# Kernel tuning notes

Hardware: AMD Instinct MI355X
Metric: run time of the kernel (lower is better)

The kernel has to match this reference:

```python
import jax, jax.numpy as jnp
import numpy as np

L, B, H, D, S, FF = 24, 4, 16, 512, 4096, 2048
HD = D // H
POS = 2048  # current kv_cache_len (write position)
EPS = 1e-5
SCALE = 1.0 / np.sqrt(HD)


def layer_norm(x, w, b):
    m = jnp.mean(x, axis=-1, keepdims=True)
    v = jnp.mean(jnp.square(x - m), axis=-1, keepdims=True)
    return (x - m) * jax.lax.rsqrt(v + EPS) * w + b


def setup_inputs() -> dict:
    key = jax.random.key(0)
    ks = jax.random.split(key, 12)
    f = lambda k, shape: jax.random.normal(k, shape, dtype=jnp.float32) * 0.02
    # decode mask: positions [0, POS] are attendable (index_fill_ sets POS True)
    attn_mask = jnp.broadcast_to(jnp.arange(S) <= POS, (B, H, 1, S))
    return {
        "x": jax.random.normal(ks[0], (B, 1, D), dtype=jnp.float32),
        "k_cache": jax.random.normal(ks[1], (L, B, H, S, HD), dtype=jnp.float32),
        "v_cache": jax.random.normal(ks[2], (L, B, H, S, HD), dtype=jnp.float32),
        "attn_mask": attn_mask,
        "qkv_w": f(ks[3], (L, 3 * D, D)),
        "qkv_b": f(ks[4], (L, 3 * D)),
        "out_w": f(ks[5], (L, D, D)),
        "out_b": f(ks[6], (L, D)),
        "mlp_w1": f(ks[7], (L, FF, D)),
        "mlp_b1": f(ks[8], (L, FF)),
        "mlp_w2": f(ks[9], (L, D, FF)),
        "mlp_b2": f(ks[10], (L, D)),
        "norm_w1": jnp.ones((L, D), jnp.float32),
        "norm_b1": jnp.zeros((L, D), jnp.float32),
        "norm_w2": jnp.ones((L, D), jnp.float32),
        "norm_b2": jnp.zeros((L, D), jnp.float32),
        "kv_cache_len": POS,
    }


def reference(x, k_cache, v_cache, attn_mask, qkv_w, qkv_b, out_w, out_b,
              mlp_w1, mlp_b1, mlp_w2, mlp_b2, norm_w1, norm_b1, norm_w2,
              norm_b2, kv_cache_len):
    pos = kv_cache_len

    def block(h, p):
        kc0, vc0, qw, qb, ow, ob, w1, b1, w2, b2, nw1, nb1, nw2, nb2 = p
        qkv = h @ qw.T + qb                      # [B,1,3D]
        q, k, v = jnp.split(qkv, 3, axis=-1)
        q = q.reshape(B, 1, H, HD).transpose(0, 2, 1, 3)   # [B,H,1,HD]
        k = k.reshape(B, 1, H, HD).transpose(0, 2, 1, 3)
        v = v.reshape(B, 1, H, HD).transpose(0, 2, 1, 3)
        # in-place cache update at write position (index_copy_ on dim 2)
        kc = kc0.at[:, :, pos, :].set(k[:, :, 0, :])       # [B,H,S,HD]
        vc = vc0.at[:, :, pos, :].set(v[:, :, 0, :])
        scores = jnp.einsum('bhqd,bhkd->bhqk', q, kc) * SCALE
        scores = jnp.where(attn_mask, scores, -1e9)
        attn = jnp.einsum('bhqk,bhkd->bhqd', jax.nn.softmax(scores, axis=-1), vc)
        attn = attn.transpose(0, 2, 1, 3).reshape(B, 1, D)
        attn = attn @ ow.T + ob
        h = layer_norm(h + attn, nw1, nb1)
        mlp = jax.nn.relu(h @ w1.T + b1) @ w2.T + b2
        h = layer_norm(h + mlp, nw2, nb2)
        return h, None

    xs = (k_cache, v_cache, qkv_w, qkv_b, out_w, out_b, mlp_w1, mlp_b1,
          mlp_w2, mlp_b2, norm_w1, norm_b1, norm_w2, norm_b2)
    out, _ = jax.lax.scan(block, x, xs)
    return out
```

## Files before the change

kernel.cpp:

```cpp
#include <hip/hip_runtime.h>


#define DEV __device__ __forceinline__

static constexpr int LNUM = 24;
static constexpr int B = 4;
static constexpr int H = 16;
static constexpr int D = 512;
static constexpr int S = 4096;
static constexpr int FF = 2048;
static constexpr int HD = 32;
static constexpr int NCH = 9;
static constexpr int NBLK = 512;
static constexpr float EPS = 1e-5f;
static constexpr float SCALE = 0.17677669529663687f;

DEV float dot4(float4 a, float4 b) { return a.x*b.x + a.y*b.y + a.z*b.z + a.w*b.w; }

DEV float gld(const float* p) {
    return __hip_atomic_load((float*)p, __ATOMIC_RELAXED, __HIP_MEMORY_SCOPE_AGENT);
}
DEV void gst(float* p, float v) {
    __hip_atomic_store(p, v, __ATOMIC_RELAXED, __HIP_MEMORY_SCOPE_AGENT);
}

DEV float waveReduceSum(float v) {
#pragma unroll
    for (int o = 32; o > 0; o >>= 1) v += __shfl_xor(v, o);
    return v;
}
DEV float waveReduceMax(float v) {
#pragma unroll
    for (int o = 32; o > 0; o >>= 1) v = fmaxf(v, __shfl_xor(v, o));
    return v;
}
DEV float blockReduceSum(float v, volatile float* red) {
    v = waveReduceSum(v);
    __syncthreads();
    if ((threadIdx.x & 63) == 0) red[threadIdx.x >> 6] = v;
    __syncthreads();
    return red[0] + red[1] + red[2] + red[3];
}
DEV float blockReduceMax(float v, volatile float* red) {
    v = waveReduceMax(v);
    __syncthreads();
    if ((threadIdx.x & 63) == 0) red[threadIdx.x >> 6] = v;
    __syncthreads();
    return fmaxf(fmaxf(red[0], red[1]), fmaxf(red[2], red[3]));
}

DEV void g_arrive(unsigned* sub, unsigned* root, unsigned subTarget) {
    __syncthreads();
    if (threadIdx.x == 0) {
        unsigned old = __hip_atomic_fetch_add(sub, 1u, __ATOMIC_RELAXED,
                                              __HIP_MEMORY_SCOPE_AGENT);
        if (old == subTarget - 1u)
            __hip_atomic_fetch_add(root, 1u, __ATOMIC_RELAXED,
                                   __HIP_MEMORY_SCOPE_AGENT);
    }
}
DEV void g_wait(unsigned* root, unsigned rootTarget) {
    if (threadIdx.x == 0) {
        while (__hip_atomic_load(root, __ATOMIC_RELAXED,
                                 __HIP_MEMORY_SCOPE_AGENT) < rootTarget)
            __builtin_amdgcn_s_sleep(1);
    }
    __syncthreads();
}

struct Params {
    const float *x, *kc, *vc;
    const float *qkvw, *qkvb, *outw, *outb, *w1, *b1, *w2, *b2;
    const float *nw1, *nb1, *nw2, *nb2;
    const int* posp;
    float *part, *t1, *m1, *sbuf, *out;
    unsigned* bar;
};

__global__ __launch_bounds__(256, 2) void mega(Params p) {
    const int blk = blockIdx.x;
    const int b = blk >> 7;
    const int gblk = blk & 127;
    const int tid = threadIdx.x;
    const int w = tid >> 6;
    const int lane = tid & 63;
    const int pos = p.posp[0];

    __shared__ float SM[2308];
    float* red = SM + 2304;

    float* partg = p.part + b * 4352;
    float* t1g   = p.t1 + (b << 9);
    float* m1g   = p.m1 + (b << 11);
    float* sbufg = p.sbuf + (b << 9);
    unsigned* root = p.bar + (size_t)b * 512;
    unsigned* sub  = root + 32 + (gblk >> 4) * 32;
    unsigned nb_ = 0;

    const int h = gblk >> 3, c = gblk & 7;
    const int bh = (b << 4) + h;

    for (int l = 0; l < LNUM; ++l) {
        const float* hsrc = (l == 0) ? (p.x + (b << 9)) : sbufg;
        const bool aln = (l > 0);
        const float* pnw = p.nw2 + (aln ? (size_t)(l - 1) * 512 : 0);
        const float* pnb = p.nb2 + (aln ? (size_t)(l - 1) * 512 : 0);
        const float* qwL = p.qkvw + (size_t)l * 1536 * 512;
        const float* qbL = p.qkvb + (size_t)l * 1536;
        const float* kcL = p.kc + (size_t)l * 8388608;
        const float* vcL = p.vc + (size_t)l * 8388608;
        const float* owL = p.outw + (size_t)l * 512 * 512;
        const float* obL = p.outb + (size_t)l * 512;
        const float* w1L = p.w1 + (size_t)l * 2048 * 512;
        const float* b1L = p.b1 + (size_t)l * 2048;
        const float* w2L = p.w2 + (size_t)l * 512 * 2048;
        const float* b2L = p.b2 + (size_t)l * 512;
        const float* n1w = p.nw1 + (size_t)l * 512;
        const float* n1b = p.nb1 + (size_t)l * 512;

        {
            const int pp2 = (c << 8) + tid;
            float4 kpre[8];
            {
                const float4* kp = (const float4*)(kcL + ((size_t)bh * 4096 + pp2) * 32);
#pragma unroll
                for (int i = 0; i < 8; ++i) kpre[i] = kp[i];
            }
            float vpre[32];
            {
                const float* vp = vcL + ((size_t)bh * 4096 + (c << 8) + ((tid >> 5) << 5)) * 32 + (tid & 31);
#pragma unroll
                for (int i = 0; i < 32; ++i) vpre[i] = vp[(size_t)i * 32];
            }
            if (l) g_wait(root, nb_ * 8);

            float a0 = gld(hsrc + tid), a1 = gld(hsrc + tid + 256);
            float s = blockReduceSum(a0 + a1, red);
            float s2 = blockReduceSum(a0 * a0 + a1 * a1, red);
            float mean = s * (1.f / 512.f);
            float rs = rsqrtf(s2 * (1.f / 512.f) - mean * mean + EPS);
            if (aln) {
                SM[tid] = (a0 - mean) * rs * pnw[tid] + pnb[tid];
                SM[tid + 256] = (a1 - mean) * rs * pnw[tid + 256] + pnb[tid + 256];
            } else {
                SM[tid] = a0;
                SM[tid + 256] = a1;
            }
            __syncthreads();

            const int qd = tid >> 3, s8 = tid & 7;
            {
                const float4* wr = (const float4*)(qwL + (size_t)((h << 5) + qd) * 512) + s8 * 16;
                const float4* hh4 = (const float4*)SM + s8 * 16;
                float a = 0.f;
#pragma unroll
                for (int i = 0; i < 16; ++i) a += dot4(wr[i], hh4[i]);
                a += __shfl_xor(a, 1); a += __shfl_xor(a, 2); a += __shfl_xor(a, 4);
                if (s8 == 0) SM[1032 + qd] = (a + qbL[(h << 5) + qd]) * SCALE;
            }
            if (c == 7) {
                {
                    const float4* wr = (const float4*)(qwL + (size_t)(512 + (h << 5) + qd) * 512) + s8 * 16;
                    const float4* hh4 = (const float4*)SM + s8 * 16;
                    float a = 0.f;
#pragma unroll
                    for (int i = 0; i < 16; ++i) a += dot4(wr[i], hh4[i]);
                    a += __shfl_xor(a, 1); a += __shfl_xor(a, 2); a += __shfl_xor(a, 4);
                    if (s8 == 0) SM[1064 + qd] = a + qbL[512 + (h << 5) + qd];
                }
                {
                    const float4* wr = (const float4*)(qwL + (size_t)(1024 + (h << 5) + qd) * 512) + s8 * 16;
                    const float4* hh4 = (const float4*)SM + s8 * 16;
                    float a = 0.f;
#pragma unroll
                    for (int i = 0; i < 16; ++i) a += dot4(wr[i], hh4[i]);
                    a += __shfl_xor(a, 1); a += __shfl_xor(a, 2); a += __shfl_xor(a, 4);
                    if (s8 == 0) SM[1096 + qd] = a + qbL[1024 + (h << 5) + qd];
                }
            }
            __syncthreads();

            float* qs = SM + 1032;
            float sc = 0.f;
#pragma unroll
            for (int i = 0; i < 8; ++i)
                sc += qs[4 * i] * kpre[i].x + qs[4 * i + 1] * kpre[i].y
                    + qs[4 * i + 2] * kpre[i].z + qs[4 * i + 3] * kpre[i].w;
            const bool act = pp2 < pos;
            float score = act ? sc : -1e30f;
            float smax = score, snew = 0.f;
            if (c == 7 && tid == 0) {
                for (int j = 0; j < 32; ++j) snew += qs[j] * SM[1064 + j];
                smax = fmaxf(smax, snew);
            }
            float m = blockReduceMax(smax, red);
            if (tid == 0) SM[1128] = (c == 7) ? expf(snew - m) : 0.f;
            float e = act ? expf(score - m) : 0.f;
            SM[512 + tid] = e;
            float lsum = blockReduceSum(e, red) + SM[1128];

            const int d = tid & 31, g = tid >> 5;
            float acc = 0.f;
#pragma unroll
            for (int i = 0; i < 32; ++i) acc += SM[512 + (g << 5) + i] * vpre[i];
            if (c == 7 && g == 0) acc += SM[1128] * SM[1096 + d];
            SM[768 + g * 33 + d] = acc;
            __syncthreads();
            if (tid < 32) {
                float o = 0.f;
#pragma unroll
                for (int gg = 0; gg < 8; ++gg) o += SM[768 + gg * 33 + tid];
                float* pt = partg + (size_t)((h << 3) + c) * 34;
                gst(pt + 2 + tid, o);
                if (tid == 0) { gst(pt + 0, m); gst(pt + 1, lsum); }
            }
            g_arrive(sub, root, (nb_ + 1) * 16); ++nb_;
        }

        {
            const int dd = (gblk << 2) + w;
            float4 oA, oB;
            {
                const float4* wr4 = (const float4*)(owL + (size_t)dd * 512);
                oA = wr4[lane]; oB = wr4[lane + 64];
            }
            float a0 = gld(hsrc + tid), a1 = gld(hsrc + tid + 256);
            g_wait(root, nb_ * 8);

            if (tid < 16) {
                const float* pt = partg + (size_t)(tid << 3) * 34;
                float mh = -1e30f;
                float mv[8];
#pragma unroll
                for (int cc = 0; cc < 8; ++cc) { mv[cc] = gld(pt + cc * 34); mh = fmaxf(mh, mv[cc]); }
                float ssum = 0.f;
#pragma unroll
                for (int cc = 0; cc < 8; ++cc) ssum += gld(pt + cc * 34 + 1) * expf(mv[cc] - mh);
                SM[512 + tid] = mh;
                SM[528 + tid] = ssum;
            }
            __syncthreads();
#pragma unroll
            for (int k = 0; k < 2; ++k) {
                int e = tid + (k << 8);
                int h2 = e >> 5, d2 = e & 31;
                const float* pt = partg + (size_t)(h2 << 3) * 34;
                float mh = SM[512 + h2];
                float inv = 1.f / SM[528 + h2];
                float o = 0.f;
#pragma unroll
                for (int cc = 0; cc < 8; ++cc)
                    o += gld(pt + cc * 34 + 2 + d2) * expf(gld(pt + cc * 34) - mh);
                SM[e] = o * inv;
            }
            float s = blockReduceSum(a0 + a1, red);
            float s2 = blockReduceSum(a0 * a0 + a1 * a1, red);
            float mean = s * (1.f / 512.f);
            float rs = rsqrtf(s2 * (1.f / 512.f) - mean * mean + EPS);
            __syncthreads();
            const float4* as4 = (const float4*)SM;
            float acc = dot4(oA, as4[lane]) + dot4(oB, as4[lane + 64]);
            acc = waveReduceSum(acc);
            if (lane == 0) {
                float hv = gld(hsrc + dd);
                if (aln) hv = (hv - mean) * rs * pnw[dd] + pnb[dd];
                gst(t1g + dd, hv + acc + obL[dd]);
            }
            g_arrive(sub, root, (nb_ + 1) * 16); ++nb_;
        }

        {
            const int rr = (gblk << 4) + (tid >> 4);
            const int s16 = tid & 15;
            float4 w1pre[8];
            {
                const float4* wr = (const float4*)(w1L + (size_t)rr * 512) + s16 * 8;
#pragma unroll
                for (int i = 0; i < 8; ++i) w1pre[i] = wr[i];
            }
            float g0 = n1w[tid], g1 = n1w[tid + 256];
            float be0 = n1b[tid], be1 = n1b[tid + 256];
            float bv = b1L[rr];
            g_wait(root, nb_ * 8);

            float a0 = gld(t1g + tid), a1 = gld(t1g + tid + 256);
            float s = blockReduceSum(a0 + a1, red);
            float s2 = blockReduceSum(a0 * a0 + a1 * a1, red);
            float mean = s * (1.f / 512.f);
            float rs = rsqrtf(s2 * (1.f / 512.f) - mean * mean + EPS);
            SM[tid] = (a0 - mean) * rs * g0 + be0;
            SM[tid + 256] = (a1 - mean) * rs * g1 + be1;
            __syncthreads();
            const float4* hh4 = (const float4*)SM + s16 * 8;
            float a = 0.f;
#pragma unroll
            for (int i = 0; i < 8; ++i) a += dot4(w1pre[i], hh4[i]);
            a += __shfl_xor(a, 1); a += __shfl_xor(a, 2);
            a += __shfl_xor(a, 4); a += __shfl_xor(a, 8);
            if (s16 == 0) gst(m1g + rr, fmaxf(a + bv, 0.f));
            g_arrive(sub, root, (nb_ + 1) * 16); ++nb_;
        }

        {
            const int dd = (gblk << 2) + w;
            float4 w2pre[8];
            {
                const float4* wr4 = (const float4*)(w2L + (size_t)dd * 2048);
#pragma unroll
                for (int i = 0; i < 8; ++i) w2pre[i] = wr4[(i << 6) + lane];
            }
            float a0 = gld(t1g + tid), a1 = gld(t1g + tid + 256);
            float tv = 0.f, gw = 0.f, gb = 0.f, bv = 0.f;
            if (lane == 0) { tv = gld(t1g + dd); gw = n1w[dd]; gb = n1b[dd]; bv = b2L[dd]; }
            g_wait(root, nb_ * 8);

#pragma unroll
            for (int i = 0; i < 8; ++i) SM[tid + (i << 8)] = gld(m1g + tid + (i << 8));
            float s = blockReduceSum(a0 + a1, red);
            float s2 = blockReduceSum(a0 * a0 + a1 * a1, red);
            float mean = s * (1.f / 512.f);
            float rs = rsqrtf(s2 * (1.f / 512.f) - mean * mean + EPS);
            __syncthreads();
            const float4* ms4 = (const float4*)SM;
            float acc = 0.f;
#pragma unroll
            for (int i = 0; i < 8; ++i) acc += dot4(w2pre[i], ms4[(i << 6) + lane]);
            acc = waveReduceSum(acc);
            if (lane == 0) {
                float hl = (tv - mean) * rs * gw + gb;
                gst(sbufg + dd, hl + acc + bv);
            }
            g_arrive(sub, root, (nb_ + 1) * 16); ++nb_;
        }
    }

    if (gblk == 0) {
        g_wait(root, nb_ * 8);
        const float* nw = p.nw2 + 23 * 512;
        const float* nbv = p.nb2 + 23 * 512;
        float a0 = gld(sbufg + tid), a1 = gld(sbufg + tid + 256);
        float s = blockReduceSum(a0 + a1, red);
        float s2 = blockReduceSum(a0 * a0 + a1 * a1, red);
        float mean = s * (1.f / 512.f);
        float rs = rsqrtf(s2 * (1.f / 512.f) - mean * mean + EPS);
        p.out[(b << 9) + tid] = (a0 - mean) * rs * nw[tid] + nbv[tid];
        p.out[(b << 9) + 256 + tid] = (a1 - mean) * rs * nw[tid + 256] + nbv[tid + 256];
    }
}

DEV float waveReduceSumF(float v) { return waveReduceSum(v); }

__global__ __launch_bounds__(256) void k_qkv(
    const float* __restrict__ hsrc, int apply_ln,
    const float* __restrict__ nw, const float* __restrict__ nb,
    const float* __restrict__ w, const float* __restrict__ bias,
    float* __restrict__ qkv)
{
    const int lane = threadIdx.x & 63;
    const int wid = (blockIdx.x << 2) + (threadIdx.x >> 6);
    const int b = wid / 1536;
    const int r = wid - b * 1536;
    const float* hb = hsrc + (b << 9);
    const int k0 = lane << 3;
    float4 h0 = *(const float4*)(hb + k0);
    float4 h1 = *(const float4*)(hb + k0 + 4);
    float hv[8] = {h0.x, h0.y, h0.z, h0.w, h1.x, h1.y, h1.z, h1.w};
    if (apply_ln) {
        float s = 0.f, s2 = 0.f;
#pragma unroll
        for (int j = 0; j < 8; ++j) { s += hv[j]; s2 += hv[j] * hv[j]; }
        s = waveReduceSum(s);
        s2 = waveReduceSum(s2);
        float mean = s * (1.f / 512.f);
        float rs = rsqrtf(s2 * (1.f / 512.f) - mean * mean + EPS);
        float4 nw0 = *(const float4*)(nw + k0);
        float4 nw1 = *(const float4*)(nw + k0 + 4);
        float4 nb0 = *(const float4*)(nb + k0);
        float4 nb1 = *(const float4*)(nb + k0 + 4);
        float nwv[8] = {nw0.x, nw0.y, nw0.z, nw0.w, nw1.x, nw1.y, nw1.z, nw1.w};
        float nbv[8] = {nb0.x, nb0.y, nb0.z, nb0.w, nb1.x, nb1.y, nb1.z, nb1.w};
#pragma unroll
        for (int j = 0; j < 8; ++j) hv[j] = (hv[j] - mean) * rs * nwv[j] + nbv[j];
    }
    const float* wr = w + (size_t)r * 512 + k0;
    float4 w0 = *(const float4*)(wr);
    float4 w1 = *(const float4*)(wr + 4);
    float acc = w0.x * hv[0] + w0.y * hv[1] + w0.z * hv[2] + w0.w * hv[3]
              + w1.x * hv[4] + w1.y * hv[5] + w1.z * hv[6] + w1.w * hv[7];
    acc = waveReduceSum(acc);
    if (lane == 0) {
        float v = acc + bias[r];
        if (r < 512) v *= SCALE;
        qkv[b * 1536 + r] = v;
    }
}

__global__ __launch_bounds__(256) void k_attn(
    const float* __restrict__ kc, const float* __restrict__ vc,
    const float* __restrict__ qkv, float* __restrict__ part,
    const int* __restrict__ posp)
{
    const int tid = threadIdx.x;
    const int c = blockIdx.x % NCH;
    const int bh = blockIdx.x / NCH;
    const int b = bh >> 4, h = bh & 15;
    const int pos = posp[0];
    __shared__ float qs[32];
    __shared__ float es[256];
    __shared__ float red[4];
    __shared__ float op[8][33];
    if (tid < 32) qs[tid] = qkv[b * 1536 + h * 32 + tid];
    __syncthreads();
    float score = -1e30f;
    bool act = false;
    if (c < 8) {
        int p = c * 256 + tid;
        act = (p < pos);
        const float4* kp = (const float4*)(kc + ((size_t)bh * S + p) * HD);
        float s = 0.f;
#pragma unroll
        for (int i = 0; i < 8; ++i) {
            float4 kv = kp[i];
            s += qs[4 * i] * kv.x + qs[4 * i + 1] * kv.y + qs[4 * i + 2] * kv.z + qs[4 * i + 3] * kv.w;
        }
        if (act) score = s;
    } else if (tid == 0) {
        act = true;
        const float* kp = qkv + b * 1536 + 512 + h * 32;
        float s = 0.f;
#pragma unroll
        for (int j = 0; j < 32; ++j) s += qs[j] * kp[j];
        score = s;
    }
    float m;
    {
        float v = waveReduceMax(score);
        __syncthreads();
        if ((tid & 63) == 0) red[tid >> 6] = v;
        __syncthreads();
        m = fmaxf(fmaxf(red[0], red[1]), fmaxf(red[2], red[3]));
    }
    float e = act ? expf(score - m) : 0.f;
    es[tid] = e;
    float lsum;
    {
        float v = waveReduceSum(e);
        __syncthreads();
        if ((tid & 63) == 0) red[tid >> 6] = v;
        __syncthreads();
        lsum = red[0] + red[1] + red[2] + red[3];
    }
    const int d = tid & 31, g = tid >> 5;
    float acc = 0.f;
    if (c < 8) {
        const float* vp = vc + ((size_t)bh * S + c * 256 + g * 32) * HD + d;
#pragma unroll 8
        for (int i = 0; i < 32; ++i) acc += es[g * 32 + i] * vp[(size_t)i * HD];
    } else if (g == 0) {
        acc = es[0] * qkv[b * 1536 + 1024 + h * 32 + d];
    }
    op[g][d] = acc;
    __syncthreads();
    if (tid < 32) {
        float o = 0.f;
#pragma unroll
        for (int gg = 0; gg < 8; ++gg) o += op[gg][tid];
        float* pp = part + (size_t)(bh * NCH + c) * 34;
        pp[2 + tid] = o;
        if (tid == 0) { pp[0] = m; pp[1] = lsum; }
    }
}

__global__ __launch_bounds__(256) void k_outproj(
    const float* __restrict__ part,
    const float* __restrict__ ow, const float* __restrict__ ob,
    const float* __restrict__ hsrc, int apply_ln,
    const float* __restrict__ nw, const float* __restrict__ nb,
    float* __restrict__ t1)
{
    const int tid = threadIdx.x;
    const int b = blockIdx.x >> 5;
    const int oc = blockIdx.x & 31;
    __shared__ float attn_s[512];
    __shared__ float hln[512];
    __shared__ float mh[16], sh[16];
    __shared__ float red[4];
    if (tid < 16) {
        const float* pp = part + (size_t)(b * 16 + tid) * NCH * 34;
        float m = -1e30f;
        for (int c = 0; c < NCH; ++c) m = fmaxf(m, pp[c * 34]);
        float ss = 0.f;
        for (int c = 0; c < NCH; ++c) ss += pp[c * 34 + 1] * expf(pp[c * 34] - m);
        mh[tid] = m;
        sh[tid] = ss;
    }
    __syncthreads();
#pragma unroll
    for (int e = tid; e < 512; e += 256) {
        int h = e >> 5, d = e & 31;
        const float* pp = part + (size_t)(b * 16 + h) * NCH * 34;
        float o = 0.f;
        for (int c = 0; c < NCH; ++c) o += pp[c * 34 + 2 + d] * expf(pp[c * 34] - mh[h]);
        attn_s[e] = o / sh[h];
    }
    float a0 = hsrc[(b << 9) + tid], a1 = hsrc[(b << 9) + 256 + tid];
    if (apply_ln) {
        float s = blockReduceSum(a0 + a1, red);
        float s2 = blockReduceSum(a0 * a0 + a1 * a1, red);
        float mean = s * (1.f / 512.f);
        float rs = rsqrtf(s2 * (1.f / 512.f) - mean * mean + EPS);
        hln[tid] = (a0 - mean) * rs * nw[tid] + nb[tid];
        hln[tid + 256] = (a1 - mean) * rs * nw[tid + 256] + nb[tid + 256];
    } else {
        hln[tid] = a0;
        hln[tid + 256] = a1;
    }
    __syncthreads();
    const int w = tid >> 6, lane = tid & 63, k0 = lane << 3;
#pragma unroll
    for (int oi = 0; oi < 4; ++oi) {
        int dd = (oc << 4) + (w << 2) + oi;
        const float4* wp = (const float4*)(ow + (size_t)dd * 512 + k0);
        float4 w0 = wp[0], w1 = wp[1];
        float acc = w0.x * attn_s[k0] + w0.y * attn_s[k0 + 1] + w0.z * attn_s[k0 + 2] + w0.w * attn_s[k0 + 3]
                  + w1.x * attn_s[k0 + 4] + w1.y * attn_s[k0 + 5] + w1.z * attn_s[k0 + 6] + w1.w * attn_s[k0 + 7];
        acc = waveReduceSum(acc);
        if (lane == 0) t1[(b << 9) + dd] = hln[dd] + acc + ob[dd];
    }
}

__global__ __launch_bounds__(256) void k_mlp1(
    const float* __restrict__ t1,
    const float* __restrict__ nw, const float* __restrict__ nb,
    const float* __restrict__ w1, const float* __restrict__ b1,
    float* __restrict__ m1)
{
    const int tid = threadIdx.x;
    const int b = blockIdx.x >> 7;
    const int oc = blockIdx.x & 127;
    __shared__ float hln[512];
    __shared__ float red[4];
    float a0 = t1[(b << 9) + tid], a1 = t1[(b << 9) + 256 + tid];
    float s = blockReduceSum(a0 + a1, red);
    float s2 = blockReduceSum(a0 * a0 + a1 * a1, red);
    float mean = s * (1.f / 512.f);
    float rs = rsqrtf(s2 * (1.f / 512.f) - mean * mean + EPS);
    hln[tid] = (a0 - mean) * rs * nw[tid] + nb[tid];
    hln[tid + 256] = (a1 - mean) * rs * nw[tid + 256] + nb[tid + 256];
    __syncthreads();
    const int w = tid >> 6, lane = tid & 63, k0 = lane << 3;
#pragma unroll
    for (int oi = 0; oi < 4; ++oi) {
        int r = (oc << 4) + (w << 2) + oi;
        const float4* wp = (const float4*)(w1 + (size_t)r * 512 + k0);
        float4 w0 = wp[0], w1v = wp[1];
        float acc = w0.x * hln[k0] + w0.y * hln[k0 + 1] + w0.z * hln[k0 + 2] + w0.w * hln[k0 + 3]
                  + w1v.x * hln[k0 + 4] + w1v.y * hln[k0 + 5] + w1v.z * hln[k0 + 6] + w1v.w * hln[k0 + 7];
        acc = waveReduceSum(acc);
        if (lane == 0) m1[(b << 11) + r] = fmaxf(acc + b1[r], 0.f);
    }
}

__global__ __launch_bounds__(256) void k_mlp2(
    const float* __restrict__ m1, const float* __restrict__ t1,
    const float* __restrict__ nw, const float* __restrict__ nb,
    const float* __restrict__ w2, const float* __restrict__ b2,
    float* __restrict__ sout)
{
    const int tid = threadIdx.x;
    const int b = blockIdx.x >> 7;
    const int oc = blockIdx.x & 127;
    __shared__ float ms[2048];
    __shared__ float red[4];
#pragma unroll
    for (int i = 0; i < 8; ++i) ms[tid + (i << 8)] = m1[(b << 11) + tid + (i << 8)];
    float a0 = t1[(b << 9) + tid], a1 = t1[(b << 9) + 256 + tid];
    float s = blockReduceSum(a0 + a1, red);
    float s2 = blockReduceSum(a0 * a0 + a1 * a1, red);
    float mean = s * (1.f / 512.f);
    float rs = rsqrtf(s2 * (1.f / 512.f) - mean * mean + EPS);
    const int w = tid >> 6, lane = tid & 63;
    const int dd = (oc << 2) + w;
    const float4* wp = (const float4*)(w2 + (size_t)dd * 2048);
    float acc = 0.f;
#pragma unroll
    for (int i = 0; i < 8; ++i) {
        int idx = (i << 6) + lane;
        float4 q = wp[idx];
        int k = idx << 2;
        acc += q.x * ms[k] + q.y * ms[k + 1] + q.z * ms[k + 2] + q.w * ms[k + 3];
    }
    acc = waveReduceSum(acc);
    if (lane == 0) {
        float td = t1[(b << 9) + dd];
        float hd = (td - mean) * rs * nw[dd] + nb[dd];
        sout[(b << 9) + dd] = hd + acc + b2[dd];
    }
}

__global__ __launch_bounds__(256) void k_finalln(
    const float* __restrict__ sbuf,
    const float* __restrict__ nw, const float* __restrict__ nb,
    float* __restrict__ out)
{
    const int b = blockIdx.x, tid = threadIdx.x;
    __shared__ float red[4];
    float a0 = sbuf[(b << 9) + tid], a1 = sbuf[(b << 9) + 256 + tid];
    float s = blockReduceSum(a0 + a1, red);
    float s2 = blockReduceSum(a0 * a0 + a1 * a1, red);
    float mean = s * (1.f / 512.f);
    float rs = rsqrtf(s2 * (1.f / 512.f) - mean * mean + EPS);
    out[(b << 9) + tid] = (a0 - mean) * rs * nw[tid] + nb[tid];
    out[(b << 9) + 256 + tid] = (a1 - mean) * rs * nw[tid + 256] + nb[tid + 256];
}

extern "C" void kernel_launch(void* const* d_in, const int* in_sizes, int n_in,
                              void* d_out, int out_size, void* d_ws, size_t ws_size,
                              hipStream_t stream)
{
    const float* x    = (const float*)d_in[0];
    const float* kc   = (const float*)d_in[1];
    const float* vc   = (const float*)d_in[2];
    const float* qkvw = (const float*)d_in[4];
    const float* qkvb = (const float*)d_in[5];
    const float* outw = (const float*)d_in[6];
    const float* outb = (const float*)d_in[7];
    const float* w1   = (const float*)d_in[8];
    const float* b1   = (const float*)d_in[9];
    const float* w2   = (const float*)d_in[10];
    const float* b2   = (const float*)d_in[11];
    const float* nw1  = (const float*)d_in[12];
    const float* nb1  = (const float*)d_in[13];
    const float* nw2  = (const float*)d_in[14];
    const float* nb2  = (const float*)d_in[15];
    const int*   posp = (const int*)d_in[16];

    int dev = 0, cu = 0, nb = 0;
    hipGetDevice(&dev);
    hipDeviceGetAttribute(&cu, hipDeviceAttributeMultiprocessorCount, dev);
    hipOccupancyMaxActiveBlocksPerMultiprocessor(&nb, (const void*)mega, 256, 0);
    const bool coop_ok = ((long)nb * cu >= NBLK);

    float* ws = (float*)d_ws;

    if (coop_ok) {
        Params prm;
        prm.x = x; prm.kc = kc; prm.vc = vc;
        prm.qkvw = qkvw; prm.qkvb = qkvb; prm.outw = outw; prm.outb = outb;
        prm.w1 = w1; prm.b1 = b1; prm.w2 = w2; prm.b2 = b2;
        prm.nw1 = nw1; prm.nb1 = nb1; prm.nw2 = nw2; prm.nb2 = nb2;
        prm.posp = posp;
        prm.part = ws;
        prm.t1   = prm.part + 17408;
        prm.m1   = prm.t1 + 2048;
        prm.sbuf = prm.m1 + 8192;
        prm.out  = (float*)d_out;
        prm.bar  = (unsigned*)(ws + 29696);
        hipMemsetAsync(prm.bar, 0, 8192, stream);
        void* args[] = { &prm };
        hipLaunchCooperativeKernel(reinterpret_cast<const void*>(&mega),
                                   dim3(NBLK), dim3(256), args, 0, stream);
        return;
    }

    float* qkvbuf = ws;
    float* part   = qkvbuf + 6144;
    float* t1     = part + 19584;
    float* m1     = t1 + 2048;
    float* sbuf   = m1 + 8192;
    const size_t kvLayerStride = (size_t)B * H * S * HD;

    for (int l = 0; l < LNUM; ++l) {
        const float* hsrc = (l == 0) ? x : sbuf;
        const int aln = (l > 0) ? 1 : 0;
        const float* pnw = (l > 0) ? (nw2 + (size_t)(l - 1) * 512) : nullptr;
        const float* pnb = (l > 0) ? (nb2 + (size_t)(l - 1) * 512) : nullptr;

        k_qkv<<<1536, 256, 0, stream>>>(hsrc, aln, pnw, pnb,
                                        qkvw + (size_t)l * 1536 * 512,
                                        qkvb + (size_t)l * 1536, qkvbuf);
        k_attn<<<B * H * NCH, 256, 0, stream>>>(kc + (size_t)l * kvLayerStride,
                                                vc + (size_t)l * kvLayerStride,
                                                qkvbuf, part, posp);
        k_outproj<<<B * 32, 256, 0, stream>>>(part,
                                              outw + (size_t)l * 512 * 512,
                                              outb + (size_t)l * 512,
                                              hsrc, aln, pnw, pnb, t1);
        k_mlp1<<<B * 128, 256, 0, stream>>>(t1,
                                            nw1 + (size_t)l * 512, nb1 + (size_t)l * 512,
                                            w1 + (size_t)l * FF * D, b1 + (size_t)l * FF, m1);
        k_mlp2<<<B * 128, 256, 0, stream>>>(m1, t1,
                                            nw1 + (size_t)l * 512, nb1 + (size_t)l * 512,
                                            w2 + (size_t)l * D * FF, b2 + (size_t)l * 512, sbuf);
    }
    k_finalln<<<B, 256, 0, stream>>>(sbuf, nw2 + 23 * 512, nb2 + 23 * 512, (float*)d_out);
}
```

Before: 844.6 us.

## Flatten grid barrier, drop softmax max, accumulate LayerNorm stats atomically

Replaces the two-level per-batch grid barrier with a single flat counter that all 128 blocks increment. Drops the running-max subtraction in the attention softmax and merges partial results by plain summation. Replaces per-block LayerNorm mean/variance block reductions with global atomic accumulation of sum and sum-of-squares, so each block reads the stats instead of reducing 512 values itself. This removes several __syncthreads-heavy reductions and exp rescaling per phase, but adds atomic contention on one counter and overflow risk in exp without max subtraction.

```diff
diff --git a/kernel.cpp b/kernel.cpp
--- a/kernel.cpp
+++ b/kernel.cpp
@@ -23,6 +23,9 @@
 DEV void gst(float* p, float v) {
     __hip_atomic_store(p, v, __ATOMIC_RELAXED, __HIP_MEMORY_SCOPE_AGENT);
 }
+DEV void gadd(float* p, float v) {
+    __hip_atomic_fetch_add(p, v, __ATOMIC_RELAXED, __HIP_MEMORY_SCOPE_AGENT);
+}
 
 DEV float waveReduceSum(float v) {
 #pragma unroll
@@ -49,20 +52,14 @@
     return fmaxf(fmaxf(red[0], red[1]), fmaxf(red[2], red[3]));
 }
 
-DEV void g_arrive(unsigned* sub, unsigned* root, unsigned subTarget) {
-    __syncthreads();
+DEV void g_arrive(unsigned* ctr) {
+    __syncthreads();
+    if (threadIdx.x == 0)
+        __hip_atomic_fetch_add(ctr, 1u, __ATOMIC_RELAXED, __HIP_MEMORY_SCOPE_AGENT);
+}
+DEV void g_wait(unsigned* ctr, unsigned target) {
     if (threadIdx.x == 0) {
-        unsigned old = __hip_atomic_fetch_add(sub, 1u, __ATOMIC_RELAXED,
-                                              __HIP_MEMORY_SCOPE_AGENT);
-        if (old == subTarget - 1u)
-            __hip_atomic_fetch_add(root, 1u, __ATOMIC_RELAXED,
-                                   __HIP_MEMORY_SCOPE_AGENT);
-    }
-}
-DEV void g_wait(unsigned* root, unsigned rootTarget) {
-    if (threadIdx.x == 0) {
-        while (__hip_atomic_load(root, __ATOMIC_RELAXED,
-                                 __HIP_MEMORY_SCOPE_AGENT) < rootTarget)
+        while (__hip_atomic_load(ctr, __ATOMIC_RELAXED, __HIP_MEMORY_SCOPE_AGENT) < target)
             __builtin_amdgcn_s_sleep(1);
     }
     __syncthreads();
@@ -93,8 +90,10 @@
     float* t1g   = p.t1 + (b << 9);
     float* m1g   = p.m1 + (b << 11);
     float* sbufg = p.sbuf + (b << 9);
-    unsigned* root = p.bar + (size_t)b * 512;
-    unsigned* sub  = root + 32 + (gblk >> 4) * 32;
+    unsigned* ctr = p.bar + (size_t)b * 64;
+    float* stats  = (float*)(p.bar + 256);
+    float* stT1   = stats + b * 96;
+    float* stSB   = stats + b * 96 + 48;
     unsigned nb_ = 0;
 
     const int h = gblk >> 3, c = gblk & 7;
@@ -132,14 +131,13 @@
 #pragma unroll
                 for (int i = 0; i < 32; ++i) vpre[i] = vp[(size_t)i * 32];
             }
-            if (l) g_wait(root, nb_ * 8);
+            if (l) g_wait(ctr, nb_ * 128);
 
             float a0 = gld(hsrc + tid), a1 = gld(hsrc + tid + 256);
-            float s = blockReduceSum(a0 + a1, red);
-            float s2 = blockReduceSum(a0 * a0 + a1 * a1, red);
-            float mean = s * (1.f / 512.f);
-            float rs = rsqrtf(s2 * (1.f / 512.f) - mean * mean + EPS);
             if (aln) {
+                float ss = gld(stSB + (l - 1) * 2), sq = gld(stSB + (l - 1) * 2 + 1);
+                float mean = ss * (1.f / 512.f);
+                float rs = rsqrtf(sq * (1.f / 512.f) - mean * mean + EPS);
                 SM[tid] = (a0 - mean) * rs * pnw[tid] + pnb[tid];
                 SM[tid + 256] = (a1 - mean) * rs * pnw[tid + 256] + pnb[tid + 256];
             } else {
@@ -187,17 +185,18 @@
                 sc += qs[4 * i] * kpre[i].x + qs[4 * i + 1] * kpre[i].y
                     + qs[4 * i + 2] * kpre[i].z + qs[4 * i + 3] * kpre[i].w;
             const bool act = pp2 < pos;
-            float score = act ? sc : -1e30f;
-            float smax = score, snew = 0.f;
-            if (c == 7 && tid == 0) {
-                for (int j = 0; j < 32; ++j) snew += qs[j] * SM[1064 + j];
-                smax = fmaxf(smax, snew);
-            }
-            float m = blockReduceMax(smax, red);
-            if (tid == 0) SM[1128] = (c == 7) ? expf(snew - m) : 0.f;
-            float e = act ? expf(score - m) : 0.f;
+            float e = act ? expf(sc) : 0.f;
+            if (tid == 0) {
+                float en = 0.f;
+                if (c == 7) {
+                    float snew = 0.f;
+                    for (int j = 0; j < 32; ++j) snew += qs[j] * SM[1064 + j];
+                    en = expf(snew);
+                }
+                SM[1128] = en;
+            }
             SM[512 + tid] = e;
-            float lsum = blockReduceSum(e, red) + SM[1128];
+            float den = blockReduceSum(e, red) + SM[1128];
 
             const int d = tid & 31, g = tid >> 5;
             float acc = 0.f;
@@ -211,10 +210,10 @@
 #pragma unroll
                 for (int gg = 0; gg < 8; ++gg) o += SM[768 + gg * 33 + tid];
                 float* pt = partg + (size_t)((h << 3) + c) * 34;
-                gst(pt + 2 + tid, o);
-                if (tid == 0) { gst(pt + 0, m); gst(pt + 1, lsum); }
-            }
-            g_arrive(sub, root, (nb_ + 1) * 16); ++nb_;
+                gst(pt + 1 + tid, o);
+                if (tid == 0) gst(pt, den);
+            }
+            g_arrive(ctr); ++nb_;
         }
 
         {
@@ -224,39 +223,31 @@
                 const float4* wr4 = (const float4*)(owL + (size_t)dd * 512);
                 oA = wr4[lane]; oB = wr4[lane + 64];
             }
-            float a0 = gld(hsrc + tid), a1 = gld(hsrc + tid + 256);
-            g_wait(root, nb_ * 8);
+            float mean = 0.f, rs = 1.f;
+            if (aln) {
+                float ss = gld(stSB + (l - 1) * 2), sq = gld(stSB + (l - 1) * 2 + 1);
+                mean = ss * (1.f / 512.f);
+                rs = rsqrtf(sq * (1.f / 512.f) - mean * mean + EPS);
+            }
+            g_wait(ctr, nb_ * 128);
 
             if (tid < 16) {
-                const float* pt = partg + (size_t)(tid << 3) * 34;
-                float mh = -1e30f;
-                float mv[8];
-#pragma unroll
-                for (int cc = 0; cc < 8; ++cc) { mv[cc] = gld(pt + cc * 34); mh = fmaxf(mh, mv[cc]); }
-                float ssum = 0.f;
-#pragma unroll
-                for (int cc = 0; cc < 8; ++cc) ssum += gld(pt + cc * 34 + 1) * expf(mv[cc] - mh);
-                SM[512 + tid] = mh;
-                SM[528 + tid] = ssum;
+                float dsum = 0.f;
+#pragma unroll
+                for (int cc = 0; cc < 8; ++cc) dsum += gld(partg + (size_t)((tid << 3) + cc) * 34);
+                SM[512 + tid] = 1.f / dsum;
             }
             __syncthreads();
 #pragma unroll
             for (int k = 0; k < 2; ++k) {
                 int e = tid + (k << 8);
                 int h2 = e >> 5, d2 = e & 31;
-                const float* pt = partg + (size_t)(h2 << 3) * 34;
-                float mh = SM[512 + h2];
-                float inv = 1.f / SM[528 + h2];
                 float o = 0.f;
 #pragma unroll
                 for (int cc = 0; cc < 8; ++cc)
-                    o += gld(pt + cc * 34 + 2 + d2) * expf(gld(pt + cc * 34) - mh);
-                SM[e] = o * inv;
-            }
-            float s = blockReduceSum(a0 + a1, red);
-            float s2 = blockReduceSum(a0 * a0 + a1 * a1, red);
-            float mean = s * (1.f / 512.f);
-            float rs = rsqrtf(s2 * (1.f / 512.f) - mean * mean + EPS);
+                    o += gld(partg + (size_t)((h2 << 3) + cc) * 34 + 1 + d2);
+                SM[e] = o * SM[512 + h2];
+            }
             __syncthreads();
             const float4* as4 = (const float4*)SM;
             float acc = dot4(oA, as4[lane]) + dot4(oB, as4[lane + 64]);
@@ -264,9 +255,19 @@
             if (lane == 0) {
                 float hv = gld(hsrc + dd);
                 if (aln) hv = (hv - mean) * rs * pnw[dd] + pnb[dd];
-                gst(t1g + dd, hv + acc + obL[dd]);
-            }
-            g_arrive(sub, root, (nb_ + 1) * 16); ++nb_;
+                float tv = hv + acc + obL[dd];
+                gst(t1g + dd, tv);
+                SM[1024 + w] = tv;
+            }
+            __syncthreads();
+            if (tid == 0) {
+                float s = SM[1024] + SM[1025] + SM[1026] + SM[1027];
+                float q = SM[1024] * SM[1024] + SM[1025] * SM[1025]
+                        + SM[1026] * SM[1026] + SM[1027] * SM[1027];
+                gadd(stT1 + l * 2, s);
+                gadd(stT1 + l * 2 + 1, q);
+            }
+            g_arrive(ctr); ++nb_;
         }
 
         {
@@ -281,13 +282,12 @@
             float g0 = n1w[tid], g1 = n1w[tid + 256];
             float be0 = n1b[tid], be1 = n1b[tid + 256];
             float bv = b1L[rr];
-            g_wait(root, nb_ * 8);
+            g_wait(ctr, nb_ * 128);
 
             float a0 = gld(t1g + tid), a1 = gld(t1g + tid + 256);
-            float s = blockReduceSum(a0 + a1, red);
-            float s2 = blockReduceSum(a0 * a0 + a1 * a1, red);
-            float mean = s * (1.f / 512.f);
-            float rs = rsqrtf(s2 * (1.f / 512.f) - mean * mean + EPS);
+            float ss = gld(stT1 + l * 2), sq = gld(stT1 + l * 2 + 1);
+            float mean = ss * (1.f / 512.f);
+            float rs = rsqrtf(sq * (1.f / 512.f) - mean * mean + EPS);
             SM[tid] = (a0 - mean) * rs * g0 + be0;
             SM[tid + 256] = (a1 - mean) * rs * g1 + be1;
             __syncthreads();
@@ -298,7 +298,7 @@
             a += __shfl_xor(a, 1); a += __shfl_xor(a, 2);
             a += __shfl_xor(a, 4); a += __shfl_xor(a, 8);
             if (s16 == 0) gst(m1g + rr, fmaxf(a + bv, 0.f));
-            g_arrive(sub, root, (nb_ + 1) * 16); ++nb_;
+            g_arrive(ctr); ++nb_;
         }
 
         {
@@ -309,17 +309,15 @@
 #pragma unroll
                 for (int i = 0; i < 8; ++i) w2pre[i] = wr4[(i << 6) + lane];
             }
-            float a0 = gld(t1g + tid), a1 = gld(t1g + tid + 256);
             float tv = 0.f, gw = 0.f, gb = 0.f, bv = 0.f;
             if (lane == 0) { tv = gld(t1g + dd); gw = n1w[dd]; gb = n1b[dd]; bv = b2L[dd]; }
-            g_wait(root, nb_ * 8);
+            float ss = gld(stT1 + l * 2), sq = gld(stT1 + l * 2 + 1);
+            float mean = ss * (1.f / 512.f);
+            float rs = rsqrtf(sq * (1.f / 512.f) - mean * mean + EPS);
+            g_wait(ctr, nb_ * 128);
 
 #pragma unroll
             for (int i = 0; i < 8; ++i) SM[tid + (i << 8)] = gld(m1g + tid + (i << 8));
-            float s = blockReduceSum(a0 + a1, red);
-            float s2 = blockReduceSum(a0 * a0 + a1 * a1, red);
-            float mean = s * (1.f / 512.f);
-            float rs = rsqrtf(s2 * (1.f / 512.f) - mean * mean + EPS);
             __syncthreads();
             const float4* ms4 = (const float4*)SM;
             float acc = 0.f;
@@ -328,27 +326,34 @@
             acc = waveReduceSum(acc);
             if (lane == 0) {
                 float hl = (tv - mean) * rs * gw + gb;
-                gst(sbufg + dd, hl + acc + bv);
-            }
-            g_arrive(sub, root, (nb_ + 1) * 16); ++nb_;
+                float sv = hl + acc + bv;
+                gst(sbufg + dd, sv);
+                SM[2048 + w] = sv;
+            }
+            __syncthreads();
+            if (tid == 0) {
+                float s = SM[2048] + SM[2049] + SM[2050] + SM[2051];
+                float q = SM[2048] * SM[2048] + SM[2049] * SM[2049]
+                        + SM[2050] * SM[2050] + SM[2051] * SM[2051];
+                gadd(stSB + l * 2, s);
+                gadd(stSB + l * 2 + 1, q);
+            }
+            g_arrive(ctr); ++nb_;
         }
     }
 
     if (gblk == 0) {
-        g_wait(root, nb_ * 8);
+        g_wait(ctr, nb_ * 128);
         const float* nw = p.nw2 + 23 * 512;
         const float* nbv = p.nb2 + 23 * 512;
         float a0 = gld(sbufg + tid), a1 = gld(sbufg + tid + 256);
-        float s = blockReduceSum(a0 + a1, red);
-        float s2 = blockReduceSum(a0 * a0 + a1 * a1, red);
-        float mean = s * (1.f / 512.f);
-        float rs = rsqrtf(s2 * (1.f / 512.f) - mean * mean + EPS);
+        float ss = gld(stSB + 23 * 2), sq = gld(stSB + 23 * 2 + 1);
+        float mean = ss * (1.f / 512.f);
+        float rs = rsqrtf(sq * (1.f / 512.f) - mean * mean + EPS);
         p.out[(b << 9) + tid] = (a0 - mean) * rs * nw[tid] + nbv[tid];
         p.out[(b << 9) + 256 + tid] = (a1 - mean) * rs * nw[tid + 256] + nbv[tid + 256];
     }
 }
-
-DEV float waveReduceSumF(float v) { return waveReduceSum(v); }
 
 __global__ __launch_bounds__(256) void k_qkv(
     const float* __restrict__ hsrc, int apply_ln,
@@ -432,24 +437,10 @@
         for (int j = 0; j < 32; ++j) s += qs[j] * kp[j];
         score = s;
     }
-    float m;
-    {
-        float v = waveReduceMax(score);
-        __syncthreads();
-        if ((tid & 63) == 0) red[tid >> 6] = v;
-        __syncthreads();
-        m = fmaxf(fmaxf(red[0], red[1]), fmaxf(red[2], red[3]));
-    }
+    float m = blockReduceMax(score, red);
     float e = act ? expf(score - m) : 0.f;
     es[tid] = e;
-    float lsum;
-    {
-        float v = waveReduceSum(e);
-        __syncthreads();
-        if ((tid & 63) == 0) red[tid >> 6] = v;
-        __syncthreads();
-        lsum = red[0] + red[1] + red[2] + red[3];
-    }
+    float l = blockReduceSum(e, red);
     const int d = tid & 31, g = tid >> 5;
     float acc = 0.f;
     if (c < 8) {
@@ -467,7 +458,7 @@
         for (int gg = 0; gg < 8; ++gg) o += op[gg][tid];
         float* pp = part + (size_t)(bh * NCH + c) * 34;
         pp[2 + tid] = o;
-        if (tid == 0) { pp[0] = m; pp[1] = lsum; }
+        if (tid == 0) { pp[0] = m; pp[1] = l; }
     }
 }
 
@@ -656,7 +647,7 @@
         prm.sbuf = prm.m1 + 8192;
         prm.out  = (float*)d_out;
         prm.bar  = (unsigned*)(ws + 29696);
-        hipMemsetAsync(prm.bar, 0, 8192, stream);
+        hipMemsetAsync(prm.bar, 0, 2560, stream);
         void* args[] = { &prm };
         hipLaunchCooperativeKernel(reinterpret_cast<const void*>(&mega),
                                    dim3(NBLK), dim3(256), args, 0, stream);
```

Measured after the change: 845.7 us. No clear change (+0.1%).
